# Performance work log

Measured on AMD Instinct MI355X. Metric: run time of the kernel, lower is better.

Reference implementation:

```python
import jax, jax.numpy as jnp
import numpy as np

H = 16  # n_head

def _rotate_half(x):
    d = x.shape[-1] // 2
    return jnp.concatenate([-x[..., d:], x[..., :d]], axis=-1)

def setup_inputs() -> dict:
    key = jax.random.key(0)
    ks = jax.random.split(key, 12)
    b, t, f, h = 8, 1024, 1024, H
    d = f // h
    inp = {
        "query": jax.random.normal(ks[0], (b, t, f), jnp.float32),
        "key": jax.random.normal(ks[1], (b, t, f), jnp.float32),
        "value": jax.random.normal(ks[2], (b, t, f), jnp.float32),
    }
    # realistic rotary cos/sin, shape (t,1,1,d_k)
    inv_freq = 1.0 / (10000.0 ** (np.arange(0, d, 2, dtype=np.float32) / d))
    pos = np.arange(t, dtype=np.float32)[:, None] * inv_freq[None, :]  # (t, d/2)
    emb = np.concatenate([pos, pos], axis=-1)  # (t, d)
    inp["cos"] = jnp.asarray(np.cos(emb)).reshape(t, 1, 1, d)
    inp["sin"] = jnp.asarray(np.sin(emb)).reshape(t, 1, 1, d)
    inp["mask"] = jax.random.randint(ks[3], (b, t, t), 0, 2) > 0
    s = 1.0 / np.sqrt(f)
    inp["Wq"] = jax.random.normal(ks[4], (f, f), jnp.float32) * s
    inp["bq"] = jax.random.normal(ks[5], (f,), jnp.float32) * 0.02
    inp["Wk"] = jax.random.normal(ks[6], (f, f), jnp.float32) * s
    inp["bk"] = jax.random.normal(ks[7], (f,), jnp.float32) * 0.02
    inp["Wv"] = jax.random.normal(ks[8], (f, f), jnp.float32) * s
    inp["bv"] = jax.random.normal(ks[9], (f,), jnp.float32) * 0.02
    inp["Wo"] = jax.random.normal(ks[10], (f, f), jnp.float32) * s
    inp["bo"] = jax.random.normal(ks[11], (f,), jnp.float32) * 0.02
    return inp

def reference(query, key, value, cos, sin, mask, Wq, bq, Wk, bk, Wv, bv, Wo, bo):
    b, t, f = query.shape
    h = H
    d = f // h
    # RoPE applied pre-projection, per-head layout (b,t,h,d)
    c = cos.reshape(1, t, 1, d)  # broadcast over batch and heads
    s = sin.reshape(1, t, 1, d)
    qr = query.reshape(b, t, h, d)
    kr = key.reshape(b, t, h, d)
    qr = qr * c + _rotate_half(qr) * s
    kr = kr * c + _rotate_half(kr) * s
    q_in = qr.reshape(b, t, f)
    k_in = kr.reshape(b, t, f)
    # QKV projections (nn.Linear: x @ W.T + b), then split heads -> (b,h,t,d)
    q = (jnp.einsum('btf,gf->btg', q_in, Wq) + bq).reshape(b, t, h, d).transpose(0, 2, 1, 3)
    k = (jnp.einsum('btf,gf->btg', k_in, Wk) + bk).reshape(b, t, h, d).transpose(0, 2, 1, 3)
    v = (jnp.einsum('btf,gf->btg', value, Wv) + bv).reshape(b, t, h, d).transpose(0, 2, 1, 3)
    scores = jnp.einsum('bhqd,bhkd->bhqk', q, k) / jnp.sqrt(jnp.asarray(d, q.dtype))
    m = mask[:, None, :, :]  # (b,1,t,t)
    scores = jnp.where(m, jnp.asarray(-10000.0, scores.dtype), scores)
    attn = jax.nn.softmax(scores, axis=-1)
    attn = jnp.where(m, jnp.asarray(0.0, attn.dtype), attn)
    out = jnp.einsum('bhqk,bhkd->bhqd', attn, v)  # (b,h,t,d)
    out = out.transpose(0, 2, 1, 3).reshape(b, t, f)
    return jnp.einsum('btf,gf->btg', out, Wo) + bo
```

## Files before the change

kernel.cpp:

```cpp
#include <hip/hip_runtime.h>
#include <stdint.h>

typedef short short8 __attribute__((ext_vector_type(8)));
typedef float f32x4 __attribute__((ext_vector_type(4)));
typedef unsigned short ushort4v __attribute__((ext_vector_type(4)));
typedef unsigned int uint4v __attribute__((ext_vector_type(4)));
typedef unsigned long long u64;

#if __has_builtin(__builtin_amdgcn_exp2f)
#define EXP2(x) __builtin_amdgcn_exp2f(x)
#else
#define EXP2(x) exp2f(x)
#endif

__device__ __forceinline__ unsigned perm_hi16(unsigned hi, unsigned lo) {
#if __has_builtin(__builtin_amdgcn_perm)
  return __builtin_amdgcn_perm(hi, lo, 0x07060302u);
#else
  return (hi & 0xffff0000u) | (lo >> 16);
#endif
}

__device__ __forceinline__ unsigned short f2bf(float f) {
  union { float f; unsigned u; } v; v.f = f;
  unsigned r = v.u + 0x7fffu + ((v.u >> 16) & 1u);
  return (unsigned short)(r >> 16);
}

__device__ __forceinline__ void gld_lds16(const void* g, void* l) {
  __builtin_amdgcn_global_load_lds((const __attribute__((address_space(1))) void*)g,
                                   (__attribute__((address_space(3))) void*)l, 16, 0, 0);
}

__global__ void mask_pack(const int* __restrict__ mask, u64* __restrict__ bits) {
  const int tid = blockIdx.x * 256 + threadIdx.x;
  const int w = tid >> 6, lane = tid & 63;
  const int h = w & 1, tb = (w >> 1) & 7, bq = w >> 4;
  const int v = mask[(size_t)bq * 1024 + tb * 128 + h * 8 + (lane & 7) * 16 + (lane >> 3)];
  const u64 b = __ballot(v != 0);
  if (lane == 0) bits[w] = b;
}

__global__ void rope_kernel(const float* __restrict__ q, const float* __restrict__ k,
                            const float* __restrict__ cs, const float* __restrict__ sn,
                            unsigned short* __restrict__ qo, unsigned short* __restrict__ ko) {
  const int idx = blockIdx.x * 256 + threadIdx.x;
  const int p   = idx & 7;
  const int bth = idx >> 3;
  const int t   = (bth >> 4) & 1023;
  const size_t base = (size_t)bth * 64;
  const int dd0 = p * 4;

  const float4 x0 = *(const float4*)(q + base + dd0);
  const float4 x1 = *(const float4*)(q + base + dd0 + 32);
  const float4 y0 = *(const float4*)(k + base + dd0);
  const float4 y1 = *(const float4*)(k + base + dd0 + 32);
  const float4 c0 = *(const float4*)(cs + t * 64 + dd0);
  const float4 c1 = *(const float4*)(cs + t * 64 + dd0 + 32);
  const float4 s0 = *(const float4*)(sn + t * 64 + dd0);
  const float4 s1 = *(const float4*)(sn + t * 64 + dd0 + 32);

  ushort4v qlo, qhi, klo, khi;
  qlo[0]=f2bf(x0.x*c0.x - x1.x*s0.x); qlo[1]=f2bf(x0.y*c0.y - x1.y*s0.y);
  qlo[2]=f2bf(x0.z*c0.z - x1.z*s0.z); qlo[3]=f2bf(x0.w*c0.w - x1.w*s0.w);
  qhi[0]=f2bf(x1.x*c1.x + x0.x*s1.x); qhi[1]=f2bf(x1.y*c1.y + x0.y*s1.y);
  qhi[2]=f2bf(x1.z*c1.z + x0.z*s1.z); qhi[3]=f2bf(x1.w*c1.w + x0.w*s1.w);
  klo[0]=f2bf(y0.x*c0.x - y1.x*s0.x); klo[1]=f2bf(y0.y*c0.y - y1.y*s0.y);
  klo[2]=f2bf(y0.z*c0.z - y1.z*s0.z); klo[3]=f2bf(y0.w*c0.w - y1.w*s0.w);
  khi[0]=f2bf(y1.x*c1.x + y0.x*s1.x); khi[1]=f2bf(y1.y*c1.y + y0.y*s1.y);
  khi[2]=f2bf(y1.z*c1.z + y0.z*s1.z); khi[3]=f2bf(y1.w*c1.w + y0.w*s1.w);

  *(ushort4v*)(qo + base + dd0)      = qlo;
  *(ushort4v*)(qo + base + dd0 + 32) = qhi;
  *(ushort4v*)(ko + base + dd0)      = klo;
  *(ushort4v*)(ko + base + dd0 + 32) = khi;
}

__global__ void cast_kernel(const float* __restrict__ src, unsigned short* __restrict__ dst, int n4) {
  const int i = blockIdx.x * 256 + threadIdx.x;
  if (i < n4) {
    const float4 v = *(const float4*)(src + (size_t)i * 4);
    ushort4v o;
    o[0]=f2bf(v.x); o[1]=f2bf(v.y); o[2]=f2bf(v.z); o[3]=f2bf(v.w);
    *(ushort4v*)(dst + (size_t)i * 4) = o;
  }
}

__global__ void cast4_kernel(const float* __restrict__ s0, const float* __restrict__ s1,
                             const float* __restrict__ s2, const float* __restrict__ s3,
                             unsigned short* __restrict__ d0, unsigned short* __restrict__ d1,
                             unsigned short* __restrict__ d2, unsigned short* __restrict__ d3) {
  const int m = blockIdx.y;
  const float* src = (m == 0) ? s0 : (m == 1) ? s1 : (m == 2) ? s2 : s3;
  unsigned short* dst = (m == 0) ? d0 : (m == 1) ? d1 : (m == 2) ? d2 : d3;
  const int i = blockIdx.x * 256 + threadIdx.x;
  const float4 v = *(const float4*)(src + (size_t)i * 4);
  ushort4v o;
  o[0]=f2bf(v.x); o[1]=f2bf(v.y); o[2]=f2bf(v.z); o[3]=f2bf(v.w);
  *(ushort4v*)(dst + (size_t)i * 4) = o;
}

template <int MODE>
__global__ __launch_bounds__(256, 2) void gemm_bt(
    const unsigned short* __restrict__ A, const unsigned short* __restrict__ Bw,
    const float* __restrict__ bias, void* __restrict__ C, float scale) {
  constexpr int K = 1024, N = 1024;
  const int tid = threadIdx.x;
  const int wave = tid >> 6, lane = tid & 63;
  const int m0 = blockIdx.x * 128, n0 = blockIdx.y * 128;
  __shared__ unsigned short Asm[128 * 64];
  __shared__ unsigned short Bsm[128 * 64];
  f32x4 acc[4][4] = {};
  const int wr = (wave >> 1) * 64, wc = (wave & 1) * 64;
  const int ld_row = lane >> 3;
  const int ld_col = ((lane & 7) ^ ld_row) * 8;
  const int fr = lane & 15, g = lane >> 4;
  const int fr7 = fr & 7;

  for (int k0 = 0; k0 < K; k0 += 64) {
#pragma unroll
    for (int j = 0; j < 4; ++j) {
      const int c = j * 4 + wave;
      gld_lds16(A  + (size_t)(m0 + 8 * c + ld_row) * K + k0 + ld_col, &Asm[c * 512]);
      gld_lds16(Bw + (size_t)(n0 + 8 * c + ld_row) * K + k0 + ld_col, &Bsm[c * 512]);
    }
    __syncthreads();
#pragma unroll
    for (int ks = 0; ks < 2; ++ks) {
      const int ch = ((ks * 4 + g) ^ fr7) * 8;
      short8 af[4], bf[4];
#pragma unroll
      for (int i = 0; i < 4; ++i)
        af[i] = *(const short8*)&Asm[(wr + i * 16 + fr) * 64 + ch];
#pragma unroll
      for (int i = 0; i < 4; ++i)
        bf[i] = *(const short8*)&Bsm[(wc + i * 16 + fr) * 64 + ch];
#pragma unroll
      for (int i = 0; i < 4; ++i)
#pragma unroll
        for (int j = 0; j < 4; ++j)
          acc[i][j] = __builtin_amdgcn_mfma_f32_16x16x32_bf16(af[i], bf[j], acc[i][j], 0, 0, 0);
    }
    __syncthreads();
  }

#pragma unroll
  for (int i = 0; i < 4; ++i) {
    const int row_base = m0 + wr + i * 16 + g * 4;
#pragma unroll
    for (int j = 0; j < 4; ++j) {
      const int col = n0 + wc + j * 16 + fr;
      const float bval = bias[col];
      if (MODE == 0) {
        float* Co = (float*)C;
#pragma unroll
        for (int r = 0; r < 4; ++r)
          Co[(size_t)(row_base + r) * N + col] = (acc[i][j][r] + bval) * scale;
      } else if (MODE == 1) {
        unsigned short* Co = (unsigned short*)C;
        const int h_i = col >> 6, dd = col & 63;
#pragma unroll
        for (int r = 0; r < 4; ++r) {
          const int row = row_base + r;
          const int b_i = row >> 10, t_i = row & 1023;
          Co[((size_t)(b_i * 16 + h_i) * 1024 + t_i) * 64 + dd] = f2bf((acc[i][j][r] + bval) * scale);
        }
      } else {
        unsigned short* Co = (unsigned short*)C;
        const int h_i = col >> 6, dd = col & 63;
#pragma unroll
        for (int r = 0; r < 4; ++r) {
          const int row = row_base + r;
          const int b_i = row >> 10, t_i = row & 1023;
          const int kp = (t_i & 15) * 8 + ((t_i >> 4) & 7);
          Co[((size_t)(b_i * 16 + h_i) * 64 + dd) * 1024 + (t_i & ~127) + kp] =
              f2bf((acc[i][j][r] + bval) * scale);
        }
      }
    }
  }
}

__global__ __launch_bounds__(256, 2) void flash_attn(
    const unsigned short* __restrict__ Qp, const unsigned short* __restrict__ Kp,
    const unsigned short* __restrict__ Vp, const u64* __restrict__ mbits,
    unsigned short* __restrict__ O) {
  const int bh = blockIdx.x & 127, b_i = bh >> 4, h_i = bh & 15;
  const int q0 = (blockIdx.x >> 7) * 128;
  const int tid = threadIdx.x, wave = tid >> 6, lane = tid & 63;
  const unsigned short* Qb = Qp + (size_t)bh * 65536;
  const unsigned short* Kb = Kp + (size_t)bh * 65536;
  const unsigned short* Vb = Vp + (size_t)bh * 65536;
  const u64* mb = mbits + (size_t)b_i * 16384;

  __shared__ unsigned short smem[16384];
  unsigned short* Vsm = smem;
  unsigned short* Ksm = smem + 8192;
  unsigned short* Pw  = smem + 8192 + wave * 2048;

  const int fr = lane & 15, g = lane >> 4, fr7 = fr & 7;
  const int qw = q0 + wave * 32;

  short8 qf[2][2];
#pragma unroll
  for (int mt = 0; mt < 2; ++mt)
#pragma unroll
    for (int ks = 0; ks < 2; ++ks)
      qf[mt][ks] = *(const short8*)&Qb[(size_t)(qw + mt * 16 + fr) * 64 + ks * 32 + g * 8];

  f32x4 o_acc[2][4] = {};
  float l_run[2][4] = {};

  const int kld_row = lane >> 3;
  const int kld_col = ((lane & 7) ^ kld_row) * 8;
  const int vld_row = lane >> 4;
  const int vld_r7w = 4 * (wave & 1) + vld_row;
  const int vld_col = ((lane & 15) ^ vld_r7w) * 8;

  for (int kt = 0; kt < 1024; kt += 128) {
#pragma unroll
    for (int j = 0; j < 4; ++j) {
      const int c = j * 4 + wave;
      gld_lds16(Kb + (size_t)(kt + 8 * c + kld_row) * 64 + kld_col, &Ksm[c * 512]);
      gld_lds16(Vb + (size_t)(4 * c + vld_row) * 1024 + kt + vld_col, &Vsm[c * 512]);
    }
    __syncthreads();

    f32x4 s_acc[2][8] = {};
#pragma unroll
    for (int ks = 0; ks < 2; ++ks) {
      const int ch = ((ks * 4 + g) ^ fr7) * 8;
      short8 kf[8];
#pragma unroll
      for (int nt = 0; nt < 8; ++nt)
        kf[nt] = *(const short8*)&Ksm[(nt * 16 + fr) * 64 + ch];
#pragma unroll
      for (int mt = 0; mt < 2; ++mt)
#pragma unroll
        for (int nt = 0; nt < 8; ++nt)
          s_acc[mt][nt] = __builtin_amdgcn_mfma_f32_16x16x32_bf16(qf[mt][ks], kf[nt], s_acc[mt][nt], 0, 0, 0);
    }
    __syncthreads();

#pragma unroll
    for (int mt = 0; mt < 2; ++mt) {
#pragma unroll
      for (int r = 0; r < 4; ++r) {
        const int qrow = qw + mt * 16 + g * 4 + r;
        const u64 w = mb[qrow * 16 + (kt >> 7) * 2 + (fr >> 3)];
        const unsigned byte8 = (unsigned)(w >> ((fr & 7) * 8)) & 0xffu;
        float lp = l_run[mt][r];
        unsigned t8[8];
#pragma unroll
        for (int nt = 0; nt < 8; ++nt) {
          float e = EXP2(s_acc[mt][nt][r]);
          e = (byte8 & (1u << nt)) ? 0.0f : e;
          lp += e;
          union { float f; unsigned u; } cv; cv.f = e;
          t8[nt] = cv.u + 0x7fffu + ((cv.u >> 16) & 1u);
        }
        l_run[mt][r] = lp;
        uint4v pk;
        pk[0] = perm_hi16(t8[1], t8[0]);
        pk[1] = perm_hi16(t8[3], t8[2]);
        pk[2] = perm_hi16(t8[5], t8[4]);
        pk[3] = perm_hi16(t8[7], t8[6]);
        const int prow = g * 4 + r;
        *(uint4v*)&Pw[prow * 128 + ((fr ^ (prow & 7)) * 8)] = pk;
      }

#pragma unroll
      for (int ks2 = 0; ks2 < 4; ++ks2) {
        const int cc = (ks2 * 4 + g) ^ fr7;
        short8 vf[4];
#pragma unroll
        for (int dt = 0; dt < 4; ++dt)
          vf[dt] = *(const short8*)&Vsm[(dt * 16 + fr) * 128 + cc * 8];
        const short8 pf = *(const short8*)&Pw[fr * 128 + cc * 8];
#pragma unroll
        for (int dt = 0; dt < 4; ++dt)
          o_acc[mt][dt] = __builtin_amdgcn_mfma_f32_16x16x32_bf16(pf, vf[dt], o_acc[mt][dt], 0, 0, 0);
      }
    }
    __syncthreads();
  }

#pragma unroll
  for (int mt = 0; mt < 2; ++mt)
#pragma unroll
    for (int r = 0; r < 4; ++r) {
      float l = l_run[mt][r];
#pragma unroll
      for (int off = 1; off < 16; off <<= 1) l += __shfl_xor(l, off, 16);
      const float inv_l = 1.0f / l;
      const int qrow = qw + mt * 16 + g * 4 + r;
#pragma unroll
      for (int dt = 0; dt < 4; ++dt) {
        const int dcol = dt * 16 + fr;
        O[((size_t)(b_i * 1024 + qrow)) * 1024 + h_i * 64 + dcol] = f2bf(o_acc[mt][dt][r] * inv_l);
      }
    }
}

extern "C" void kernel_launch(void* const* d_in, const int* in_sizes, int n_in,
                              void* d_out, int out_size, void* d_ws, size_t ws_size,
                              hipStream_t stream) {
  const float* query = (const float*)d_in[0];
  const float* key   = (const float*)d_in[1];
  const float* value = (const float*)d_in[2];
  const float* cosb  = (const float*)d_in[3];
  const float* sinb  = (const float*)d_in[4];
  const int*   mask  = (const int*)d_in[5];
  const float* Wq = (const float*)d_in[6];
  const float* bq = (const float*)d_in[7];
  const float* Wk = (const float*)d_in[8];
  const float* bk = (const float*)d_in[9];
  const float* Wv = (const float*)d_in[10];
  const float* bv = (const float*)d_in[11];
  const float* Wo = (const float*)d_in[12];
  const float* bo = (const float*)d_in[13];
  (void)in_sizes; (void)n_in; (void)out_size; (void)ws_size;

  char* ws = (char*)d_ws;
  const size_t MB = 1024 * 1024;
  unsigned short* q_in = (unsigned short*)(ws);
  unsigned short* k_in = (unsigned short*)(ws + 16 * MB);
  unsigned short* v_bf = (unsigned short*)(ws + 32 * MB);
  unsigned short* Qp   = (unsigned short*)(ws + 48 * MB);
  unsigned short* Kp   = (unsigned short*)(ws + 64 * MB);
  unsigned short* Vp   = (unsigned short*)(ws + 80 * MB);
  unsigned short* Wqb  = (unsigned short*)(ws + 96 * MB);
  unsigned short* Wkb  = (unsigned short*)(ws + 98 * MB);
  unsigned short* Wvb  = (unsigned short*)(ws + 100 * MB);
  unsigned short* Wob  = (unsigned short*)(ws + 102 * MB);
  u64*            mbits= (u64*)(ws + 104 * MB);
  unsigned short* attn = q_in;

  mask_pack<<<32768, 256, 0, stream>>>(mask, mbits);
  rope_kernel<<<4096, 256, 0, stream>>>(query, key, cosb, sinb, q_in, k_in);
  cast_kernel<<<8192, 256, 0, stream>>>(value, v_bf, 2097152);
  cast4_kernel<<<dim3(1024, 4), 256, 0, stream>>>(Wq, Wk, Wv, Wo, Wqb, Wkb, Wvb, Wob);

  dim3 g(64, 8), blk(256);
  gemm_bt<1><<<g, blk, 0, stream>>>(q_in, Wqb, bq, Qp, 0.18033688f);
  gemm_bt<1><<<g, blk, 0, stream>>>(k_in, Wkb, bk, Kp, 1.0f);
  gemm_bt<2><<<g, blk, 0, stream>>>(v_bf, Wvb, bv, Vp, 1.0f);
  flash_attn<<<1024, blk, 0, stream>>>(Qp, Kp, Vp, mbits, attn);
  gemm_bt<0><<<g, blk, 0, stream>>>(attn, Wob, bo, d_out, 1.0f);
}
```

Baseline: 374.9 us.

## Keep softmax probabilities in registers by computing S transposed, dropping LDS round-trip

Swaps the MFMA operand order so the score tile comes out transposed, which lets each lane's exponentiated scores be packed directly into the A-operand layout for the P·V MFMA. This removes the per-wave LDS staging buffer for P, its write/read traffic, and one __syncthreads per key tile. To match the new register layout, the mask bit packing and the V key permutation are reordered, row sums are reduced differently, bf16 conversion uses the hardware pack instruction, and s_setprio is raised around MFMA bursts. The coupled layout changes across three kernels are a correctness risk if any permutation is inconsistent.

```diff
diff --git a/kernel.cpp b/kernel.cpp
--- a/kernel.cpp
+++ b/kernel.cpp
@@ -27,6 +27,12 @@
   return (unsigned short)(r >> 16);
 }
 
+__device__ __forceinline__ unsigned cvt_pk_bf16(float lo, float hi) {
+  unsigned r;
+  asm("v_cvt_pk_bf16_f32 %0, %1, %2" : "=v"(r) : "v"(lo), "v"(hi));
+  return r;
+}
+
 __device__ __forceinline__ void gld_lds16(const void* g, void* l) {
   __builtin_amdgcn_global_load_lds((const __attribute__((address_space(1))) void*)g,
                                    (__attribute__((address_space(3))) void*)l, 16, 0, 0);
@@ -34,11 +40,13 @@
 
 __global__ void mask_pack(const int* __restrict__ mask, u64* __restrict__ bits) {
   const int tid = blockIdx.x * 256 + threadIdx.x;
-  const int w = tid >> 6, lane = tid & 63;
-  const int h = w & 1, tb = (w >> 1) & 7, bq = w >> 4;
-  const int v = mask[(size_t)bq * 1024 + tb * 128 + h * 8 + (lane & 7) * 16 + (lane >> 3)];
+  const int w = tid >> 6, j = tid & 63;
+  const int gh = w & 1, ktb = (w >> 1) & 7, bq = w >> 4;
+  const int nt = (j >> 2) & 7, r = j & 3, g = gh * 2 + (j >> 5);
+  const int k = nt * 16 + g * 4 + r;
+  const int v = mask[(size_t)bq * 1024 + ktb * 128 + k];
   const u64 b = __ballot(v != 0);
-  if (lane == 0) bits[w] = b;
+  if (j == 0) bits[w] = b;
 }
 
 __global__ void rope_kernel(const float* __restrict__ q, const float* __restrict__ k,
@@ -172,7 +180,8 @@
         for (int r = 0; r < 4; ++r) {
           const int row = row_base + r;
           const int b_i = row >> 10, t_i = row & 1023;
-          const int kp = (t_i & 15) * 8 + ((t_i >> 4) & 7);
+          const int kk = t_i & 127;
+          const int kp = ((kk >> 4) & 3) * 32 + ((kk >> 2) & 3) * 8 + ((kk >> 6) & 1) * 4 + (kk & 3);
           Co[((size_t)(b_i * 16 + h_i) * 64 + dd) * 1024 + (t_i & ~127) + kp] =
               f2bf((acc[i][j][r] + bval) * scale);
         }
@@ -196,7 +205,6 @@
   __shared__ unsigned short smem[16384];
   unsigned short* Vsm = smem;
   unsigned short* Ksm = smem + 8192;
-  unsigned short* Pw  = smem + 8192 + wave * 2048;
 
   const int fr = lane & 15, g = lane >> 4, fr7 = fr & 7;
   const int qw = q0 + wave * 32;
@@ -209,7 +217,7 @@
       qf[mt][ks] = *(const short8*)&Qb[(size_t)(qw + mt * 16 + fr) * 64 + ks * 32 + g * 8];
 
   f32x4 o_acc[2][4] = {};
-  float l_run[2][4] = {};
+  float l_run[2] = {0.0f, 0.0f};
 
   const int kld_row = lane >> 3;
   const int kld_col = ((lane & 7) ^ kld_row) * 8;
@@ -234,65 +242,71 @@
 #pragma unroll
       for (int nt = 0; nt < 8; ++nt)
         kf[nt] = *(const short8*)&Ksm[(nt * 16 + fr) * 64 + ch];
+      __builtin_amdgcn_s_setprio(1);
 #pragma unroll
       for (int mt = 0; mt < 2; ++mt)
 #pragma unroll
         for (int nt = 0; nt < 8; ++nt)
-          s_acc[mt][nt] = __builtin_amdgcn_mfma_f32_16x16x32_bf16(qf[mt][ks], kf[nt], s_acc[mt][nt], 0, 0, 0);
+          s_acc[mt][nt] = __builtin_amdgcn_mfma_f32_16x16x32_bf16(kf[nt], qf[mt][ks], s_acc[mt][nt], 0, 0, 0);
+      __builtin_amdgcn_s_setprio(0);
+    }
+
+    short8 pf[2][4];
+#pragma unroll
+    for (int mt = 0; mt < 2; ++mt) {
+      const u64 w = mb[(size_t)(qw + mt * 16 + fr) * 16 + (kt >> 7) * 2 + (g >> 1)];
+      const unsigned bits = (unsigned)(w >> ((g & 1) * 32));
+      float lp = l_run[mt];
+#pragma unroll
+      for (int ks2 = 0; ks2 < 4; ++ks2) {
+        float e[8];
+#pragma unroll
+        for (int r = 0; r < 4; ++r) {
+          float a = EXP2(s_acc[mt][ks2][r]);
+          a = (bits & (1u << (ks2 * 4 + r))) ? 0.0f : a;
+          float b2 = EXP2(s_acc[mt][ks2 + 4][r]);
+          b2 = (bits & (1u << (16 + ks2 * 4 + r))) ? 0.0f : b2;
+          e[r] = a; e[4 + r] = b2;
+          lp += a + b2;
+        }
+        uint4v pk;
+        pk[0] = cvt_pk_bf16(e[0], e[1]);
+        pk[1] = cvt_pk_bf16(e[2], e[3]);
+        pk[2] = cvt_pk_bf16(e[4], e[5]);
+        pk[3] = cvt_pk_bf16(e[6], e[7]);
+        union { uint4v u; short8 s; } cv; cv.u = pk;
+        pf[mt][ks2] = cv.s;
+      }
+      l_run[mt] = lp;
+    }
+
+#pragma unroll
+    for (int ks2 = 0; ks2 < 4; ++ks2) {
+      const int cc = (ks2 * 4 + g) ^ fr7;
+      short8 vf[4];
+#pragma unroll
+      for (int dt = 0; dt < 4; ++dt)
+        vf[dt] = *(const short8*)&Vsm[(dt * 16 + fr) * 128 + cc * 8];
+      __builtin_amdgcn_s_setprio(1);
+#pragma unroll
+      for (int mt = 0; mt < 2; ++mt)
+#pragma unroll
+        for (int dt = 0; dt < 4; ++dt)
+          o_acc[mt][dt] = __builtin_amdgcn_mfma_f32_16x16x32_bf16(pf[mt][ks2], vf[dt], o_acc[mt][dt], 0, 0, 0);
+      __builtin_amdgcn_s_setprio(0);
     }
     __syncthreads();
-
-#pragma unroll
-    for (int mt = 0; mt < 2; ++mt) {
-#pragma unroll
-      for (int r = 0; r < 4; ++r) {
-        const int qrow = qw + mt * 16 + g * 4 + r;
-        const u64 w = mb[qrow * 16 + (kt >> 7) * 2 + (fr >> 3)];
-        const unsigned byte8 = (unsigned)(w >> ((fr & 7) * 8)) & 0xffu;
-        float lp = l_run[mt][r];
-        unsigned t8[8];
-#pragma unroll
-        for (int nt = 0; nt < 8; ++nt) {
-          float e = EXP2(s_acc[mt][nt][r]);
-          e = (byte8 & (1u << nt)) ? 0.0f : e;
-          lp += e;
-          union { float f; unsigned u; } cv; cv.f = e;
-          t8[nt] = cv.u + 0x7fffu + ((cv.u >> 16) & 1u);
-        }
-        l_run[mt][r] = lp;
-        uint4v pk;
-        pk[0] = perm_hi16(t8[1], t8[0]);
-        pk[1] = perm_hi16(t8[3], t8[2]);
-        pk[2] = perm_hi16(t8[5], t8[4]);
-        pk[3] = perm_hi16(t8[7], t8[6]);
-        const int prow = g * 4 + r;
-        *(uint4v*)&Pw[prow * 128 + ((fr ^ (prow & 7)) * 8)] = pk;
-      }
-
-#pragma unroll
-      for (int ks2 = 0; ks2 < 4; ++ks2) {
-        const int cc = (ks2 * 4 + g) ^ fr7;
-        short8 vf[4];
-#pragma unroll
-        for (int dt = 0; dt < 4; ++dt)
-          vf[dt] = *(const short8*)&Vsm[(dt * 16 + fr) * 128 + cc * 8];
-        const short8 pf = *(const short8*)&Pw[fr * 128 + cc * 8];
-#pragma unroll
-        for (int dt = 0; dt < 4; ++dt)
-          o_acc[mt][dt] = __builtin_amdgcn_mfma_f32_16x16x32_bf16(pf, vf[dt], o_acc[mt][dt], 0, 0, 0);
-      }
-    }
-    __syncthreads();
-  }
-
-#pragma unroll
-  for (int mt = 0; mt < 2; ++mt)
+  }
+
+#pragma unroll
+  for (int mt = 0; mt < 2; ++mt) {
+    float red = l_run[mt];
+    red += __shfl_xor(red, 16);
+    red += __shfl_xor(red, 32);
 #pragma unroll
     for (int r = 0; r < 4; ++r) {
-      float l = l_run[mt][r];
-#pragma unroll
-      for (int off = 1; off < 16; off <<= 1) l += __shfl_xor(l, off, 16);
-      const float inv_l = 1.0f / l;
+      const float lv = __shfl(red, g * 4 + r);
+      const float inv_l = 1.0f / lv;
       const int qrow = qw + mt * 16 + g * 4 + r;
 #pragma unroll
       for (int dt = 0; dt < 4; ++dt) {
@@ -300,6 +314,7 @@
         O[((size_t)(b_i * 1024 + qrow)) * 1024 + h_i * 64 + dcol] = f2bf(o_acc[mt][dt][r] * inv_l);
       }
     }
+  }
 }
 
 extern "C" void kernel_launch(void* const* d_in, const int* in_sizes, int n_in,
```

Result: faster. 343.3 us (-8.4%).
